# Kernel optimization log

Measured on AMD Instinct MI355X. Metric: run time of the kernel, lower is better.

Reference implementation:

```python
import jax, jax.numpy as jnp
import numpy as np

N_NODES = 4096
N_EDGES = 524288
IN_DIM = 6
EMB_N = 4
EMB_D = 8
EDGE_D = 1
HID = 64
N_HEADS = 4
LN_EPS = 1e-5


def _layernorm(h, g, b):
    m = jnp.mean(h, axis=-1, keepdims=True)
    v = jnp.mean(jnp.square(h - m), axis=-1, keepdims=True)
    return (h - m) * jax.lax.rsqrt(v + LN_EPS) * g + b


def setup_inputs() -> dict:
    key = jax.random.key(0)
    ks = jax.random.split(key, 16)
    s = lambda fan_in: 1.0 / np.sqrt(fan_in)
    inp = {
        'x': jax.random.normal(ks[0], (N_NODES, IN_DIM), jnp.float32),
        'edge_attr': jax.random.uniform(ks[1], (N_EDGES, EDGE_D), jnp.float32),
        'entity_emb': jax.random.normal(ks[2], (EMB_N, EMB_D), jnp.float32),
        'lin1_w': jax.random.uniform(ks[3], (HID, IN_DIM + EMB_D + EDGE_D), jnp.float32, -s(15), s(15)),
        'lin1_b': jnp.zeros((HID,), jnp.float32),
        'lay_w': jax.random.uniform(ks[4], (HID, HID), jnp.float32, -s(HID), s(HID)),
        'lay_b': jnp.zeros((HID,), jnp.float32),
        'ln_g': jnp.ones((HID,), jnp.float32),
        'ln_b': jnp.zeros((HID,), jnp.float32),
        'in_proj_w': jax.random.uniform(ks[5], (3 * HID, HID), jnp.float32, -s(HID), s(HID)),
        'in_proj_b': jnp.zeros((3 * HID,), jnp.float32),
        'out_proj_w': jax.random.uniform(ks[6], (HID, HID), jnp.float32, -s(HID), s(HID)),
        'out_proj_b': jnp.zeros((HID,), jnp.float32),
        'an_g': jnp.ones((HID,), jnp.float32),
        'an_b': jnp.zeros((HID,), jnp.float32),
        'out_w': jax.random.uniform(ks[7], (HID, HID), jnp.float32, -s(HID), s(HID)),
        'out_b': jnp.zeros((HID,), jnp.float32),
        'edge_index': jax.random.randint(ks[8], (2, N_EDGES), 0, N_NODES, jnp.int64),
        'entity_type': jax.random.randint(ks[9], (N_NODES,), 0, EMB_N, jnp.int64),
    }
    return inp


def reference(x, edge_attr, entity_emb, lin1_w, lin1_b, lay_w, lay_b, ln_g, ln_b,
              in_proj_w, in_proj_b, out_proj_w, out_proj_b, an_g, an_b, out_w, out_b,
              edge_index, entity_type):
    # --- EmbedConv ---
    # concat node features with entity embedding: [N, 6+8]
    xe = jnp.concatenate([x, entity_emb[entity_type]], axis=-1)
    src, dst = edge_index[0], edge_index[1]
    # gather source nodes + edge attr: [E, 15]
    msg = jnp.concatenate([xe[src], edge_attr], axis=-1)
    msg = _layernorm(jax.nn.relu(msg @ lin1_w.T + lin1_b), ln_g, ln_b)
    # layer_N = 1 extra layer, shared LayerNorm
    msg = _layernorm(jax.nn.relu(msg @ lay_w.T + lay_b), ln_g, ln_b)
    # scatter-add aggregate into destination nodes: [N, 64]
    h = jax.ops.segment_sum(msg, dst, num_segments=N_NODES)
    # --- MultiheadAttention over all nodes as one sequence (eval: no dropout) ---
    qkv = h @ in_proj_w.T + in_proj_b  # [N, 3H]
    q, k, v = jnp.split(qkv, 3, axis=-1)
    hd = HID // N_HEADS
    q = q.reshape(N_NODES, N_HEADS, hd).transpose(1, 0, 2)  # [h, n, d]
    k = k.reshape(N_NODES, N_HEADS, hd).transpose(1, 0, 2)
    v = v.reshape(N_NODES, N_HEADS, hd).transpose(1, 0, 2)
    scores = jnp.einsum('hnd,hmd->hnm', q, k) / np.sqrt(hd)
    attn = jax.nn.softmax(scores, axis=-1)
    o = jnp.einsum('hnm,hmd->hnd', attn, v).transpose(1, 0, 2).reshape(N_NODES, HID)
    o = o @ out_proj_w.T + out_proj_b
    h = _layernorm(h + o, an_g, an_b)
    # --- output layer ---
    return h @ out_w.T + out_b
```

## Files before the change

kernel.cpp:

```cpp
#include <hip/hip_runtime.h>

#define N_NODES 4096
#define N_EDGES 524288
#define HID 64

typedef short short8 __attribute__((ext_vector_type(8)));
typedef float f32x4 __attribute__((ext_vector_type(4)));

__device__ __forceinline__ float bcastf(float v, int l) {
    return __int_as_float(__builtin_amdgcn_readlane(__float_as_int(v), l));
}

__device__ __forceinline__ void wave_sum2(float& a, float& b) {
    #pragma unroll
    for (int off = 32; off > 0; off >>= 1) {
        a += __shfl_xor(a, off, 64);
        b += __shfl_xor(b, off, 64);
    }
}

__device__ __forceinline__ short f2bf(float f) {
    unsigned u = __float_as_uint(f);
    u = u + 0x7FFFu + ((u >> 16) & 1u);
    return (short)(u >> 16);
}
__device__ __forceinline__ float bf2f(short s) {
    return __uint_as_float(((unsigned)(unsigned short)s) << 16);
}
__device__ __forceinline__ void split_cheap(float f, short& hi, short& lo) {
    unsigned u = __float_as_uint(f);
    unsigned hb = u & 0xffff0000u;
    float lof = f - __uint_as_float(hb);
    hi = (short)(u >> 16);
    lo = (short)(__float_as_uint(lof) >> 16);
}

__global__ void hist_prep(const float* __restrict__ x, const float* __restrict__ emb,
                          const int* __restrict__ etype, const int* __restrict__ ei,
                          const float* __restrict__ w1, const float* __restrict__ b1,
                          const float* __restrict__ w2, const float* __restrict__ lng,
                          const float* __restrict__ lnb, const float* __restrict__ b2,
                          const float* __restrict__ ipw,
                          float* __restrict__ A1, int* __restrict__ cnt, int* __restrict__ rank,
                          unsigned short* __restrict__ w2fh, unsigned short* __restrict__ w2fl,
                          unsigned short* __restrict__ ipfh, unsigned short* __restrict__ ipfl,
                          float* __restrict__ b2p) {
    int tid = blockIdx.x * 256 + threadIdx.x;
    int d = ei[N_EDGES + tid];
    rank[tid] = atomicAdd(&cnt[d], 1);
    if (tid < N_NODES * 64) {
        int n = tid >> 6, f = tid & 63;
        const float* wr = w1 + f * 15;
        float acc = b1[f];
        #pragma unroll
        for (int k = 0; k < 6; k++) acc = fmaf(x[n * 6 + k], wr[k], acc);
        int e = etype[n];
        #pragma unroll
        for (int k = 0; k < 8; k++) acc = fmaf(emb[e * 8 + k], wr[6 + k], acc);
        A1[tid] = acc;
    }
    if (tid < 4096) {
        int idx = tid >> 9, ln = (tid >> 3) & 63, j = tid & 7;
        int mm = ln & 15, qq = ln >> 4;
        int g = idx >> 1, tt = idx & 1;
        int col = tt * 32 + qq * 8 + j;
        float w = w2[(g * 16 + mm) * 64 + col] * lng[col];
        short hi = f2bf(w);
        w2fh[tid] = (unsigned short)hi;
        w2fl[tid] = (unsigned short)f2bf(w - bf2f(hi));
    }
    if (tid < 12288) {
        int idx = tid >> 9, ln = (tid >> 3) & 63, j = tid & 7;
        int mm = ln & 15, qq = ln >> 4;
        int og = idx >> 1, tt = idx & 1;
        float w = ipw[(og * 16 + mm) * 64 + tt * 32 + qq * 8 + j];
        short hi = f2bf(w);
        ipfh[tid] = (unsigned short)hi;
        ipfl[tid] = (unsigned short)f2bf(w - bf2f(hi));
    }
    if (tid < 64) {
        float acc = b2[tid];
        for (int c = 0; c < 64; c++) acc = fmaf(w2[tid * 64 + c], lnb[c], acc);
        b2p[tid] = acc;
    }
}

__global__ void __launch_bounds__(256) scatter_scan(
        const int* __restrict__ cnt, const int* __restrict__ ei,
        const float* __restrict__ edge_attr, const int* __restrict__ rank,
        int* __restrict__ bnd,
        int* __restrict__ ssrc, float* __restrict__ sea) {
    __shared__ int lbnd[4096];
    __shared__ int wsum[4];
    int t = threadIdx.x;
    int base = t * 16;
    int v16[16];
    int T = 0;
    #pragma unroll
    for (int j = 0; j < 16; j++) { v16[j] = cnt[base + j]; T += v16[j]; }
    int inc = T;
    int l = t & 63;
    #pragma unroll
    for (int off = 1; off < 64; off <<= 1) {
        int v = __shfl_up(inc, off, 64);
        if (l >= off) inc += v;
    }
    if (l == 63) wsum[t >> 6] = inc;
    __syncthreads();
    int wo = 0;
    for (int w = 0; w < (t >> 6); w++) wo += wsum[w];
    int run = wo + inc - T;
    #pragma unroll
    for (int j = 0; j < 16; j++) {
        lbnd[base + j] = run;
        run += v16[j];
    }
    if (blockIdx.x == 0) {
        #pragma unroll
        for (int j = 0; j < 16; j++) bnd[base + j] = lbnd[base + j];
        if (t == 255) bnd[4096] = run;
    }
    __syncthreads();
    int e = blockIdx.x * 256 + t;
    int d = ei[N_EDGES + e];
    int pos = lbnd[d] + rank[e];
    ssrc[pos] = ei[e];
    sea[pos] = edge_attr[e];
}

__global__ void __launch_bounds__(256, 4) edge_gather_mfma(
        const float* __restrict__ A1,
        const int* __restrict__ ssrc, const float* __restrict__ sea,
        const int* __restrict__ bnd,
        const unsigned short* __restrict__ w2fh, const unsigned short* __restrict__ w2fl,
        const float* __restrict__ w1, const float* __restrict__ b2p,
        const float* __restrict__ lg, const float* __restrict__ lb,
        float* __restrict__ h) {
    __shared__ uint4 lw2h4[512];
    __shared__ uint4 lw2l4[512];
    __shared__ float hpart[4][64];
    int tid = threadIdx.x;
    {
        const uint4* gh = (const uint4*)w2fh;
        const uint4* gl = (const uint4*)w2fl;
        lw2h4[tid] = gh[tid];
        lw2h4[tid + 256] = gh[tid + 256];
        lw2l4[tid] = gl[tid];
        lw2l4[tid + 256] = gl[tid + 256];
    }
    const unsigned short* lw2h = (const unsigned short*)lw2h4;
    const unsigned short* lw2l = (const unsigned short*)lw2l4;

    int lane = tid & 63;
    int wv = tid >> 6;
    int m = lane & 15;
    int q = lane >> 4;

    float w14f[16];
    #pragma unroll
    for (int t2 = 0; t2 < 2; t2++)
        #pragma unroll
        for (int j = 0; j < 8; j++)
            w14f[t2 * 8 + j] = w1[(t2 * 32 + q * 8 + j) * 15 + 14];
    float b2v[4];
    #pragma unroll
    for (int g = 0; g < 4; g++) b2v[g] = b2p[g * 16 + m];

    int node = blockIdx.x;
    int start = bnd[node], end = bnd[node + 1];
    int ntiles = (end - start + 15) >> 4;
    float acc[4] = {0.f, 0.f, 0.f, 0.f};
    __syncthreads();

    for (int t = wv; t < ntiles; t += 4) {
        int base = start + t * 16;
        int e = base + m;
        int ec = (e < end) ? e : (end - 1);
        int srcn = ssrc[ec];
        float eav = sea[ec];
        const float* ar = A1 + srcn * 64 + q * 8;
        float4 va = *(const float4*)(ar);
        float4 vb = *(const float4*)(ar + 4);
        float4 vc = *(const float4*)(ar + 32);
        float4 vd = *(const float4*)(ar + 36);
        float v[16] = {va.x, va.y, va.z, va.w, vb.x, vb.y, vb.z, vb.w,
                       vc.x, vc.y, vc.z, vc.w, vd.x, vd.y, vd.z, vd.w};
        float s = 0.f, s2 = 0.f;
        #pragma unroll
        for (int j = 0; j < 16; j++) {
            float u = fmaxf(fmaf(w14f[j], eav, v[j]), 0.f);
            v[j] = u;
            s += u;
            s2 = fmaf(u, u, s2);
        }
        s += __shfl_xor(s, 16, 64);  s2 += __shfl_xor(s2, 16, 64);
        s += __shfl_xor(s, 32, 64);  s2 += __shfl_xor(s2, 32, 64);
        float mean = s * (1.f / 64.f);
        float var = s2 * (1.f / 64.f) - mean * mean;
        float rs = rsqrtf(var + 1e-5f);
        float a0 = -mean * rs;
        short8 a2h[2], a2l[2];
        #pragma unroll
        for (int t2 = 0; t2 < 2; t2++)
            #pragma unroll
            for (int j = 0; j < 8; j++) {
                short hi, lo;
                split_cheap(fmaf(v[t2 * 8 + j], rs, a0), hi, lo);
                a2h[t2][j] = hi;
                a2l[t2][j] = lo;
            }
        int ob = (t >> 20);
        float s_[4] = {0, 0, 0, 0}, s2_[4] = {0, 0, 0, 0};
        float t2v[4][4];
        #pragma unroll
        for (int g = 0; g < 4; g++) {
            f32x4 c = {0.f, 0.f, 0.f, 0.f};
            #pragma unroll
            for (int t2 = 0; t2 < 2; t2++) {
                short8 bh = *(const short8*)(lw2h + ((g * 2 + t2) * 64 + lane + ob) * 8);
                short8 bl = *(const short8*)(lw2l + ((g * 2 + t2) * 64 + lane + ob) * 8);
                c = __builtin_amdgcn_mfma_f32_16x16x32_bf16(a2l[t2], bh, c, 0, 0, 0);
                c = __builtin_amdgcn_mfma_f32_16x16x32_bf16(a2h[t2], bl, c, 0, 0, 0);
                c = __builtin_amdgcn_mfma_f32_16x16x32_bf16(a2h[t2], bh, c, 0, 0, 0);
            }
            #pragma unroll
            for (int i = 0; i < 4; i++) {
                float vv = fmaxf(c[i] + b2v[g], 0.f);
                t2v[g][i] = vv;
                s_[i] += vv;
                s2_[i] = fmaf(vv, vv, s2_[i]);
            }
        }
        #pragma unroll
        for (int off = 1; off < 16; off <<= 1)
            #pragma unroll
            for (int i = 0; i < 4; i++) {
                s_[i] += __shfl_xor(s_[i], off, 64);
                s2_[i] += __shfl_xor(s2_[i], off, 64);
            }
        #pragma unroll
        for (int i = 0; i < 4; i++) {
            float mean2 = s_[i] * (1.f / 64.f);
            float var2 = s2_[i] * (1.f / 64.f) - mean2 * mean2;
            float rs2 = rsqrtf(var2 + 1e-5f);
            bool valid = (base + q * 4 + i) < end;
            #pragma unroll
            for (int g = 0; g < 4; g++) {
                float z = (t2v[g][i] - mean2) * rs2;
                if (valid) acc[g] += z;
            }
        }
    }
    #pragma unroll
    for (int g = 0; g < 4; g++) {
        acc[g] += __shfl_xor(acc[g], 16, 64);
        acc[g] += __shfl_xor(acc[g], 32, 64);
    }
    float a01 = (q & 1) ? acc[1] : acc[0];
    float a23 = (q & 1) ? acc[3] : acc[2];
    float av = (q & 2) ? a23 : a01;
    hpart[wv][q * 16 + m] = av;
    __syncthreads();
    if (tid < 64) {
        float sum = hpart[0][tid] + hpart[1][tid] + hpart[2][tid] + hpart[3][tid];
        h[node * 64 + tid] = lg[tid] * sum + (float)(end - start) * lb[tid];
    }
}

__global__ void __launch_bounds__(256) qkv_mfma(
        const float* __restrict__ h, const float* __restrict__ b,
        const unsigned short* __restrict__ ipfh, const unsigned short* __restrict__ ipfl,
        unsigned short* __restrict__ qhp, unsigned short* __restrict__ qlp,
        unsigned short* __restrict__ khp, unsigned short* __restrict__ klp,
        unsigned short* __restrict__ vT) {
    int lane = threadIdx.x & 63;
    int wv = threadIdx.x >> 6;
    int m = lane & 15;
    int q = lane >> 4;
    int wid = blockIdx.x * 4 + wv;
    int tile = wid / 12;
    int og = wid - tile * 12;
    short8 bh[2], bl[2];
    #pragma unroll
    for (int t = 0; t < 2; t++) {
        bh[t] = *(const short8*)(ipfh + ((og * 2 + t) * 64 + lane) * 8);
        bl[t] = *(const short8*)(ipfl + ((og * 2 + t) * 64 + lane) * 8);
    }
    f32x4 c = {0.f, 0.f, 0.f, 0.f};
    #pragma unroll
    for (int t = 0; t < 2; t++) {
        const float* hr = h + (tile * 16 + m) * 64 + t * 32 + q * 8;
        float4 f0 = *(const float4*)hr;
        float4 f1 = *(const float4*)(hr + 4);
        float av8[8] = {f0.x, f0.y, f0.z, f0.w, f1.x, f1.y, f1.z, f1.w};
        short8 ah, al;
        #pragma unroll
        for (int j = 0; j < 8; j++) {
            short hi, lo;
            split_cheap(av8[j], hi, lo);
            ah[j] = hi;
            al[j] = lo;
        }
        c = __builtin_amdgcn_mfma_f32_16x16x32_bf16(al, bh[t], c, 0, 0, 0);
        c = __builtin_amdgcn_mfma_f32_16x16x32_bf16(ah, bl[t], c, 0, 0, 0);
        c = __builtin_amdgcn_mfma_f32_16x16x32_bf16(ah, bh[t], c, 0, 0, 0);
    }
    int o = og * 16 + m;
    float bias = b[o];
    #pragma unroll
    for (int r = 0; r < 4; r++) {
        int node = tile * 16 + q * 4 + r;
        float val = c[r] + bias;
        if (og < 4) {
            float aq = val * (0.25f * 1.44269504f);
            size_t idx = ((size_t)(og * N_NODES + node)) * 16 + m;
            short hi = f2bf(aq);
            qhp[idx] = (unsigned short)hi;
            qlp[idx] = (unsigned short)f2bf(aq - bf2f(hi));
        } else if (og < 8) {
            size_t idx = ((size_t)((og - 4) * N_NODES + node)) * 16 + m;
            short hi = f2bf(val);
            khp[idx] = (unsigned short)hi;
            klp[idx] = (unsigned short)f2bf(val - bf2f(hi));
        } else {
            int feat = (og - 8) * 16 + m;
            vT[(size_t)feat * N_NODES + node] = (unsigned short)f2bf(val);
        }
    }
}

__global__ void __launch_bounds__(256) attn_mfma(
        const unsigned short* __restrict__ qhp, const unsigned short* __restrict__ qlp,
        const unsigned short* __restrict__ khp, const unsigned short* __restrict__ klp,
        const unsigned short* __restrict__ vT,
        float* __restrict__ part_o, float* __restrict__ part_ml) {
    __shared__ unsigned short Pl[4][16 * 72];
    int lane = threadIdx.x & 63;
    int wv = threadIdx.x >> 6;
    int m = lane & 15;
    int g = lane >> 4;
    unsigned short* Pw = Pl[wv];
    const short8 vones = {0x3F80, 0x3F80, 0x3F80, 0x3F80, 0x3F80, 0x3F80, 0x3F80, 0x3F80};

    int wid = blockIdx.x * 4 + wv;
    int kc = wid & 7;
    int qt = (wid >> 3) & 255;
    int head = wid >> 11;

    short8 aqh = (short8)0, aql = (short8)0;
    if (g < 2) {
        size_t qi = ((size_t)(head * N_NODES + qt * 16 + m)) * 16 + g * 8;
        aqh = *(const short8*)(qhp + qi);
        aql = *(const short8*)(qlp + qi);
    }
    float mS[4], lS[4];
    #pragma unroll
    for (int r = 0; r < 4; r++) { mS[r] = -3e38f; lS[r] = 0.f; }
    f32x4 Ot = {0.f, 0.f, 0.f, 0.f};

    const unsigned short* khb = khp + (size_t)head * N_NODES * 16;
    const unsigned short* klb = klp + (size_t)head * N_NODES * 16;
    const unsigned short* vtb = vT + (size_t)(head * 16 + m) * N_NODES;

    for (int bblk = 0; bblk < 8; bblk++) {
        int n0 = kc * 512 + bblk * 64;
        f32x4 S[4];
        #pragma unroll
        for (int s = 0; s < 4; s++) {
            short8 bkh = (short8)0, bkl = (short8)0;
            if (g < 2) {
                size_t ki = ((size_t)(n0 + s * 16 + m)) * 16 + g * 8;
                bkh = *(const short8*)(khb + ki);
                bkl = *(const short8*)(klb + ki);
            }
            f32x4 c = {0.f, 0.f, 0.f, 0.f};
            c = __builtin_amdgcn_mfma_f32_16x16x32_bf16(aqh, bkl, c, 0, 0, 0);
            c = __builtin_amdgcn_mfma_f32_16x16x32_bf16(aql, bkh, c, 0, 0, 0);
            c = __builtin_amdgcn_mfma_f32_16x16x32_bf16(aqh, bkh, c, 0, 0, 0);
            S[s] = c;
        }
        float mr[4];
        #pragma unroll
        for (int r = 0; r < 4; r++)
            mr[r] = fmaxf(fmaxf(S[0][r], S[1][r]), fmaxf(S[2][r], S[3][r]));
        #pragma unroll
        for (int off = 1; off < 16; off <<= 1)
            #pragma unroll
            for (int r = 0; r < 4; r++) mr[r] = fmaxf(mr[r], __shfl_xor(mr[r], off, 64));
        float alpha[4];
        #pragma unroll
        for (int r = 0; r < 4; r++) {
            float mn = fmaxf(mS[r], mr[r]);
            alpha[r] = exp2f(mS[r] - mn);
            mS[r] = mn;
        }
        #pragma unroll
        for (int s = 0; s < 4; s++) {
            #pragma unroll
            for (int r = 0; r < 4; r++) {
                float p = exp2f(S[s][r] - mS[r]);
                Pw[(g * 4 + r) * 72 + s * 16 + m] = (unsigned short)f2bf(p);
            }
        }
        #pragma unroll
        for (int r = 0; r < 4; r++) lS[r] *= alpha[r];
        int sel = lane & 3;
        float a01 = (sel & 1) ? alpha[1] : alpha[0];
        float a23 = (sel & 1) ? alpha[3] : alpha[2];
        float aown = (sel & 2) ? a23 : a01;
        int srcl = ((m >> 2) << 4) | (m & 3);
        float ab = __int_as_float(__builtin_amdgcn_ds_bpermute(srcl << 2, __float_as_int(aown)));
        #pragma unroll
        for (int r = 0; r < 4; r++) Ot[r] *= ab;
        f32x4 cl = {0.f, 0.f, 0.f, 0.f};
        #pragma unroll
        for (int t = 0; t < 2; t++) {
            short8 avf = *(const short8*)(vtb + n0 + t * 32 + g * 8);
            short8 bpf = *(const short8*)(Pw + m * 72 + t * 32 + g * 8);
            cl = __builtin_amdgcn_mfma_f32_16x16x32_bf16(vones, bpf, cl, 0, 0, 0);
            Ot = __builtin_amdgcn_mfma_f32_16x16x32_bf16(avf, bpf, Ot, 0, 0, 0);
        }
        #pragma unroll
        for (int r = 0; r < 4; r++) {
            float rsum = __int_as_float(
                __builtin_amdgcn_ds_bpermute((g * 4 + r) << 2, __float_as_int(cl[0])));
            lS[r] += rsum;
        }
    }
    size_t pb = ((size_t)(head * 8 + kc) * 256 + qt) * 256;
    *(f32x4*)(part_o + pb + m * 16 + g * 4) = Ot;
    if (m == 0) {
        size_t mb = ((size_t)(head * 8 + kc) * 256 + qt) * 32;
        #pragma unroll
        for (int r = 0; r < 4; r++) {
            part_ml[mb + g * 4 + r] = mS[r];
            part_ml[mb + 16 + g * 4 + r] = lS[r];
        }
    }
}

__global__ void post_kernel(const float* __restrict__ h,
                            const float* __restrict__ part_o, const float* __restrict__ part_ml,
                            const float* __restrict__ opw, const float* __restrict__ opb,
                            const float* __restrict__ ag, const float* __restrict__ ab,
                            const float* __restrict__ ow, const float* __restrict__ ob,
                            float* __restrict__ out) {
    __shared__ float wl1[64 * 65];
    __shared__ float wl2[64 * 65];
    for (int i = threadIdx.x; i < 4096; i += blockDim.x) {
        int r = i >> 6, c = i & 63;
        wl1[r * 65 + c] = opw[i];
        wl2[r * 65 + c] = ow[i];
    }
    __syncthreads();
    int lane = threadIdx.x & 63;
    int n = blockIdx.x * 4 + (threadIdx.x >> 6);
    int j = lane;
    int head = j >> 4, d = j & 15;
    int qt = n >> 4, qi = n & 15;
    float M = -3e38f, L = 0.f, Ov = 0.f;
    #pragma unroll
    for (int c = 0; c < 8; c++) {
        size_t base = ((size_t)(head * 8 + c) * 256 + qt);
        float mc = part_ml[base * 32 + qi];
        float lc = part_ml[base * 32 + 16 + qi];
        float ov = part_o[base * 256 + qi * 16 + d];
        if (mc > M) {
            float sc = exp2f(M - mc);
            M = mc;
            L = L * sc + lc;
            Ov = Ov * sc + ov;
        } else {
            float sc = exp2f(mc - M);
            L = fmaf(lc, sc, L);
            Ov = fmaf(ov, sc, Ov);
        }
    }
    float oj = Ov / L;
    float acc = opb[j];
    #pragma unroll
    for (int k = 0; k < 64; k++) acc = fmaf(wl1[j * 65 + k], bcastf(oj, k), acc);
    float r = h[n * 64 + j] + acc;
    float s = r, s2 = r * r;
    wave_sum2(s, s2);
    float mean = s * (1.f / 64.f);
    float var = s2 * (1.f / 64.f) - mean * mean;
    float hn = (r - mean) * rsqrtf(var + 1e-5f) * ag[j] + ab[j];
    float acc2 = ob[j];
    #pragma unroll
    for (int k = 0; k < 64; k++) acc2 = fmaf(wl2[j * 65 + k], bcastf(hn, k), acc2);
    out[n * 64 + j] = acc2;
}

extern "C" void kernel_launch(void* const* d_in, const int* in_sizes, int n_in,
                              void* d_out, int out_size, void* d_ws, size_t ws_size,
                              hipStream_t stream) {
    const float* x        = (const float*)d_in[0];
    const float* edge_attr= (const float*)d_in[1];
    const float* emb      = (const float*)d_in[2];
    const float* lin1_w   = (const float*)d_in[3];
    const float* lin1_b   = (const float*)d_in[4];
    const float* lay_w    = (const float*)d_in[5];
    const float* lay_b    = (const float*)d_in[6];
    const float* ln_g     = (const float*)d_in[7];
    const float* ln_b     = (const float*)d_in[8];
    const float* ipw      = (const float*)d_in[9];
    const float* ipb      = (const float*)d_in[10];
    const float* opw      = (const float*)d_in[11];
    const float* opb      = (const float*)d_in[12];
    const float* ang      = (const float*)d_in[13];
    const float* anb      = (const float*)d_in[14];
    const float* ow       = (const float*)d_in[15];
    const float* ob       = (const float*)d_in[16];
    const int*   ei       = (const int*)d_in[17];
    const int*   et       = (const int*)d_in[18];

    char* wsb = (char*)d_ws;
    size_t off = 0;
    float* A1             = (float*)(wsb + off);          off += 1048576;
    float* h              = (float*)(wsb + off);          off += 1048576;
    unsigned short* qhp   = (unsigned short*)(wsb + off); off += 524288;
    unsigned short* qlp   = (unsigned short*)(wsb + off); off += 524288;
    unsigned short* khp   = (unsigned short*)(wsb + off); off += 524288;
    unsigned short* klp   = (unsigned short*)(wsb + off); off += 524288;
    unsigned short* vT    = (unsigned short*)(wsb + off); off += 524288;
    float* part_o         = (float*)(wsb + off);          off += 8388608;
    float* part_ml        = (float*)(wsb + off);          off += 1048576;
    int*   cnt            = (int*)(wsb + off);            off += 16384;
    int*   bnd            = (int*)(wsb + off);            off += 16388;
    off = (off + 255) & ~(size_t)255;
    int*   rank           = (int*)(wsb + off);            off += 2097152;
    int*   ssrc           = (int*)(wsb + off);            off += 2097152;
    float* sea            = (float*)(wsb + off);          off += 2097152;
    unsigned short* w2fh  = (unsigned short*)(wsb + off); off += 8192;
    unsigned short* w2fl  = (unsigned short*)(wsb + off); off += 8192;
    unsigned short* ipfh  = (unsigned short*)(wsb + off); off += 24576;
    unsigned short* ipfl  = (unsigned short*)(wsb + off); off += 24576;
    float* b2p            = (float*)(wsb + off);          off += 256;

    (void)hipMemsetAsync(cnt, 0, 4096 * sizeof(int), stream);
    hist_prep<<<2048, 256, 0, stream>>>(x, emb, et, ei, lin1_w, lin1_b, lay_w, ln_g, ln_b,
                                        lay_b, ipw, A1, cnt, rank, w2fh, w2fl, ipfh, ipfl, b2p);
    scatter_scan<<<2048, 256, 0, stream>>>(cnt, ei, edge_attr, rank, bnd, ssrc, sea);
    edge_gather_mfma<<<4096, 256, 0, stream>>>(A1, ssrc, sea, bnd, w2fh, w2fl,
                                               lin1_w, b2p, ln_g, ln_b, h);
    qkv_mfma<<<768, 256, 0, stream>>>(h, ipb, ipfh, ipfl, qhp, qlp, khp, klp, vT);
    attn_mfma<<<2048, 256, 0, stream>>>(qhp, qlp, khp, klp, vT, part_o, part_ml);
    post_kernel<<<1024, 256, 0, stream>>>(h, part_o, part_ml, opw, opb, ang, anb, ow, ob,
                                          (float*)d_out);
}
```

Measured before the change: 242.2 us.

## Rewrite attention inner loop with 32x32 MFMA and register-resident P

Attention now uses 32x32x16 bf16 MFMA tiles. S is computed transposed, so each lane holds one query column, and the per-row max needs only a single cross-half shuffle. Probabilities are packed with v_cvt_pk_bf16_f32 and rearranged with v_permlane32_swap instead of going through LDS. The row sum comes from a ones row placed in the V operand, and the rescale is skipped when no max changed. This removes the LDS round-trip, bpermutes and multi-step reductions, and halves the grid, at the cost of different MFMA shapes and reliance on gfx950-specific instructions.

```diff
diff --git a/kernel.cpp b/kernel.cpp
--- a/kernel.cpp
+++ b/kernel.cpp
@@ -6,6 +6,7 @@
 
 typedef short short8 __attribute__((ext_vector_type(8)));
 typedef float f32x4 __attribute__((ext_vector_type(4)));
+typedef float f32x16 __attribute__((ext_vector_type(16)));
 
 __device__ __forceinline__ float bcastf(float v, int l) {
     return __int_as_float(__builtin_amdgcn_readlane(__float_as_int(v), l));
@@ -334,108 +335,93 @@
         const unsigned short* __restrict__ khp, const unsigned short* __restrict__ klp,
         const unsigned short* __restrict__ vT,
         float* __restrict__ part_o, float* __restrict__ part_ml) {
-    __shared__ unsigned short Pl[4][16 * 72];
     int lane = threadIdx.x & 63;
     int wv = threadIdx.x >> 6;
-    int m = lane & 15;
-    int g = lane >> 4;
-    unsigned short* Pw = Pl[wv];
+    int l31 = lane & 31;
+    int hi = lane >> 5;
     const short8 vones = {0x3F80, 0x3F80, 0x3F80, 0x3F80, 0x3F80, 0x3F80, 0x3F80, 0x3F80};
 
     int wid = blockIdx.x * 4 + wv;
     int kc = wid & 7;
-    int qt = (wid >> 3) & 255;
-    int head = wid >> 11;
-
-    short8 aqh = (short8)0, aql = (short8)0;
-    if (g < 2) {
-        size_t qi = ((size_t)(head * N_NODES + qt * 16 + m)) * 16 + g * 8;
-        aqh = *(const short8*)(qhp + qi);
-        aql = *(const short8*)(qlp + qi);
-    }
-    float mS[4], lS[4];
-    #pragma unroll
-    for (int r = 0; r < 4; r++) { mS[r] = -3e38f; lS[r] = 0.f; }
-    f32x4 Ot = {0.f, 0.f, 0.f, 0.f};
+    int wqt = (wid >> 3) & 127;
+    int head = wid >> 10;
+
+    int qrow = wqt * 32 + l31;
+    short8 aqh = *(const short8*)(qhp + ((size_t)(head * N_NODES + qrow)) * 16 + hi * 8);
+    short8 aql = *(const short8*)(qlp + ((size_t)(head * N_NODES + qrow)) * 16 + hi * 8);
 
     const unsigned short* khb = khp + (size_t)head * N_NODES * 16;
     const unsigned short* klb = klp + (size_t)head * N_NODES * 16;
-    const unsigned short* vtb = vT + (size_t)(head * 16 + m) * N_NODES;
-
-    for (int bblk = 0; bblk < 8; bblk++) {
-        int n0 = kc * 512 + bblk * 64;
-        f32x4 S[4];
-        #pragma unroll
-        for (int s = 0; s < 4; s++) {
-            short8 bkh = (short8)0, bkl = (short8)0;
-            if (g < 2) {
-                size_t ki = ((size_t)(n0 + s * 16 + m)) * 16 + g * 8;
-                bkh = *(const short8*)(khb + ki);
-                bkl = *(const short8*)(klb + ki);
-            }
-            f32x4 c = {0.f, 0.f, 0.f, 0.f};
-            c = __builtin_amdgcn_mfma_f32_16x16x32_bf16(aqh, bkl, c, 0, 0, 0);
-            c = __builtin_amdgcn_mfma_f32_16x16x32_bf16(aql, bkh, c, 0, 0, 0);
-            c = __builtin_amdgcn_mfma_f32_16x16x32_bf16(aqh, bkh, c, 0, 0, 0);
-            S[s] = c;
-        }
-        float mr[4];
-        #pragma unroll
-        for (int r = 0; r < 4; r++)
-            mr[r] = fmaxf(fmaxf(S[0][r], S[1][r]), fmaxf(S[2][r], S[3][r]));
-        #pragma unroll
-        for (int off = 1; off < 16; off <<= 1)
+    const unsigned short* vtb = vT + (size_t)(head * 16 + (l31 & 15)) * N_NODES;
+
+    float mS = -3e38f;
+    f32x16 Ot = {0.f, 0.f, 0.f, 0.f, 0.f, 0.f, 0.f, 0.f,
+                 0.f, 0.f, 0.f, 0.f, 0.f, 0.f, 0.f, 0.f};
+
+    for (int bb = 0; bb < 16; bb++) {
+        int n0 = kc * 512 + bb * 32;
+        const unsigned short* kpb = khb + ((size_t)(n0 + l31)) * 16 + hi * 8;
+        const unsigned short* kpl = klb + ((size_t)(n0 + l31)) * 16 + hi * 8;
+        short8 bkh = *(const short8*)kpb;
+        short8 bkl = *(const short8*)kpl;
+        f32x16 S = {0.f, 0.f, 0.f, 0.f, 0.f, 0.f, 0.f, 0.f,
+                    0.f, 0.f, 0.f, 0.f, 0.f, 0.f, 0.f, 0.f};
+        S = __builtin_amdgcn_mfma_f32_32x32x16_bf16(bkh, aql, S, 0, 0, 0);
+        S = __builtin_amdgcn_mfma_f32_32x32x16_bf16(bkl, aqh, S, 0, 0, 0);
+        S = __builtin_amdgcn_mfma_f32_32x32x16_bf16(bkh, aqh, S, 0, 0, 0);
+        float mr = S[0];
+        #pragma unroll
+        for (int r = 1; r < 16; r++) mr = fmaxf(mr, S[r]);
+        mr = fmaxf(mr, __shfl_xor(mr, 32, 64));
+        if (!__all(mr <= mS)) {
+            float mn = fmaxf(mS, mr);
+            float alpha = exp2f(mS - mn);
+            mS = mn;
             #pragma unroll
-            for (int r = 0; r < 4; r++) mr[r] = fmaxf(mr[r], __shfl_xor(mr[r], off, 64));
-        float alpha[4];
-        #pragma unroll
-        for (int r = 0; r < 4; r++) {
-            float mn = fmaxf(mS[r], mr[r]);
-            alpha[r] = exp2f(mS[r] - mn);
-            mS[r] = mn;
-        }
-        #pragma unroll
-        for (int s = 0; s < 4; s++) {
-            #pragma unroll
-            for (int r = 0; r < 4; r++) {
-                float p = exp2f(S[s][r] - mS[r]);
-                Pw[(g * 4 + r) * 72 + s * 16 + m] = (unsigned short)f2bf(p);
-            }
-        }
-        #pragma unroll
-        for (int r = 0; r < 4; r++) lS[r] *= alpha[r];
-        int sel = lane & 3;
-        float a01 = (sel & 1) ? alpha[1] : alpha[0];
-        float a23 = (sel & 1) ? alpha[3] : alpha[2];
-        float aown = (sel & 2) ? a23 : a01;
-        int srcl = ((m >> 2) << 4) | (m & 3);
-        float ab = __int_as_float(__builtin_amdgcn_ds_bpermute(srcl << 2, __float_as_int(aown)));
-        #pragma unroll
-        for (int r = 0; r < 4; r++) Ot[r] *= ab;
-        f32x4 cl = {0.f, 0.f, 0.f, 0.f};
-        #pragma unroll
-        for (int t = 0; t < 2; t++) {
-            short8 avf = *(const short8*)(vtb + n0 + t * 32 + g * 8);
-            short8 bpf = *(const short8*)(Pw + m * 72 + t * 32 + g * 8);
-            cl = __builtin_amdgcn_mfma_f32_16x16x32_bf16(vones, bpf, cl, 0, 0, 0);
-            Ot = __builtin_amdgcn_mfma_f32_16x16x32_bf16(avf, bpf, Ot, 0, 0, 0);
-        }
-        #pragma unroll
-        for (int r = 0; r < 4; r++) {
-            float rsum = __int_as_float(
-                __builtin_amdgcn_ds_bpermute((g * 4 + r) << 2, __float_as_int(cl[0])));
-            lS[r] += rsum;
-        }
-    }
-    size_t pb = ((size_t)(head * 8 + kc) * 256 + qt) * 256;
-    *(f32x4*)(part_o + pb + m * 16 + g * 4) = Ot;
-    if (m == 0) {
-        size_t mb = ((size_t)(head * 8 + kc) * 256 + qt) * 32;
-        #pragma unroll
-        for (int r = 0; r < 4; r++) {
-            part_ml[mb + g * 4 + r] = mS[r];
-            part_ml[mb + 16 + g * 4 + r] = lS[r];
-        }
+            for (int r = 0; r < 9; r++) Ot[r] *= alpha;
+        }
+        float p[16];
+        #pragma unroll
+        for (int r = 0; r < 16; r++) p[r] = exp2f(S[r] - mS);
+        unsigned w0, w1, w2, w3, u0, u1, u2, u3;
+        asm("v_cvt_pk_bf16_f32 %0, %1, %2" : "=v"(w0) : "v"(p[0]), "v"(p[1]));
+        asm("v_cvt_pk_bf16_f32 %0, %1, %2" : "=v"(w1) : "v"(p[2]), "v"(p[3]));
+        asm("v_cvt_pk_bf16_f32 %0, %1, %2" : "=v"(w2) : "v"(p[4]), "v"(p[5]));
+        asm("v_cvt_pk_bf16_f32 %0, %1, %2" : "=v"(w3) : "v"(p[6]), "v"(p[7]));
+        asm("v_cvt_pk_bf16_f32 %0, %1, %2" : "=v"(u0) : "v"(p[8]), "v"(p[9]));
+        asm("v_cvt_pk_bf16_f32 %0, %1, %2" : "=v"(u1) : "v"(p[10]), "v"(p[11]));
+        asm("v_cvt_pk_bf16_f32 %0, %1, %2" : "=v"(u2) : "v"(p[12]), "v"(p[13]));
+        asm("v_cvt_pk_bf16_f32 %0, %1, %2" : "=v"(u3) : "v"(p[14]), "v"(p[15]));
+        asm("v_permlane32_swap_b32 %0, %1" : "+v"(w0), "+v"(w2));
+        asm("v_permlane32_swap_b32 %0, %1" : "+v"(w1), "+v"(w3));
+        asm("v_permlane32_swap_b32 %0, %1" : "+v"(u0), "+v"(u2));
+        asm("v_permlane32_swap_b32 %0, %1" : "+v"(u1), "+v"(u3));
+        union { unsigned u[4]; short8 s; } pf0, pf1;
+        pf0.u[0] = w0; pf0.u[1] = w1; pf0.u[2] = w2; pf0.u[3] = w3;
+        pf1.u[0] = u0; pf1.u[1] = u1; pf1.u[2] = u2; pf1.u[3] = u3;
+        short8 v0, v1;
+        if (l31 < 16) {
+            v0 = *(const short8*)(vtb + n0 + hi * 8);
+            v1 = *(const short8*)(vtb + n0 + 16 + hi * 8);
+        } else if (l31 == 16) {
+            v0 = vones; v1 = vones;
+        } else {
+            v0 = (short8)0; v1 = (short8)0;
+        }
+        Ot = __builtin_amdgcn_mfma_f32_32x32x16_bf16(v0, pf0.s, Ot, 0, 0, 0);
+        Ot = __builtin_amdgcn_mfma_f32_32x32x16_bf16(v1, pf1.s, Ot, 0, 0, 0);
+    }
+    int qt16 = wqt * 2 + (l31 >> 4);
+    int qi = l31 & 15;
+    size_t pb = ((size_t)(head * 8 + kc) * 256 + qt16) * 256;
+    f32x4 o0 = {Ot[0], Ot[1], Ot[2], Ot[3]};
+    f32x4 o1 = {Ot[4], Ot[5], Ot[6], Ot[7]};
+    *(f32x4*)(part_o + pb + qi * 16 + hi * 4) = o0;
+    *(f32x4*)(part_o + pb + qi * 16 + 8 + hi * 4) = o1;
+    if (lane < 32) {
+        size_t mb = ((size_t)(head * 8 + kc) * 256 + qt16) * 32;
+        part_ml[mb + qi] = mS;
+        part_ml[mb + 16 + qi] = Ot[8];
     }
 }
 
@@ -545,7 +531,7 @@
     edge_gather_mfma<<<4096, 256, 0, stream>>>(A1, ssrc, sea, bnd, w2fh, w2fl,
                                                lin1_w, b2p, ln_g, ln_b, h);
     qkv_mfma<<<768, 256, 0, stream>>>(h, ipb, ipfh, ipfl, qhp, qlp, khp, klp, vT);
-    attn_mfma<<<2048, 256, 0, stream>>>(qhp, qlp, khp, klp, vT, part_o, part_ml);
+    attn_mfma<<<1024, 256, 0, stream>>>(qhp, qlp, khp, klp, vT, part_o, part_ml);
     post_kernel<<<1024, 256, 0, stream>>>(h, part_o, part_ml, opw, opb, ang, anb, ow, ob,
                                           (float*)d_out);
 }
```

Measured after the change: 227.2 us. 6.2% less time.
